# Kernel optimization log

Hardware: AMD Instinct MI355X
Metric: run time of the kernel (lower is better)

Reference implementation:

```python
import jax, jax.numpy as jnp
import numpy as np

DIM = 128
DEPTHS = 2
D_STATE = 16
D_CONV = 4
D_INNER = 2 * DIM          # expand=2
DT_RANK = DIM // 16        # ceil(128/16)=8


def layer_norm(x, g, b, eps=1e-5):
    mu = jnp.mean(x, axis=-1, keepdims=True)
    var = jnp.var(x, axis=-1, keepdims=True)
    return (x - mu) * jax.lax.rsqrt(var + eps) * g + b


def mamba_mixer(x, in_w, conv_w, conv_b, x_proj_w, dt_w, dt_b, A_log, Dp, out_w):
    # x: (B, L, DIM)
    Bb, L, _ = x.shape
    xz = x @ in_w                                  # (B, L, 2*D_INNER)
    xp, z = jnp.split(xz, 2, axis=-1)
    # causal depthwise conv1d over L (mamba: conv1d(padding=K-1)[..., :L])
    xpad = jnp.pad(xp, ((0, 0), (D_CONV - 1, 0), (0, 0)))
    xc = sum(xpad[:, k:k + L, :] * conv_w[:, k] for k in range(D_CONV)) + conv_b
    xc = jax.nn.silu(xc)
    x_dbl = xc @ x_proj_w                          # (B, L, DT_RANK + 2*D_STATE)
    dt = x_dbl[..., :DT_RANK]
    Bm = x_dbl[..., DT_RANK:DT_RANK + D_STATE]
    Cm = x_dbl[..., DT_RANK + D_STATE:]
    dt = jax.nn.softplus(dt @ dt_w + dt_b)         # (B, L, D_INNER)
    A = -jnp.exp(A_log)                            # (D_INNER, D_STATE)

    def step(h, inp):
        dt_t, B_t, C_t, x_t = inp                  # (B,di) (B,ds) (B,ds) (B,di)
        dA = jnp.exp(dt_t[:, :, None] * A)         # (B, di, ds)
        h = h * dA + (dt_t * x_t)[:, :, None] * B_t[:, None, :]
        y = jnp.einsum('bds,bs->bd', h, C_t)
        return h, y

    h0 = jnp.zeros((Bb, D_INNER, D_STATE), x.dtype)
    xs = (dt.transpose(1, 0, 2), Bm.transpose(1, 0, 2),
          Cm.transpose(1, 0, 2), xc.transpose(1, 0, 2))
    _, ys = jax.lax.scan(step, h0, xs)             # ys: (L, B, di)
    y = ys.transpose(1, 0, 2) + xc * Dp
    y = y * jax.nn.silu(z)
    return y @ out_w                               # (B, L, DIM)


def reference(x, skip, expand_w, pe_g, pe_b, ln_g, ln_b, in_proj_w, conv_w,
              conv_b, x_proj_w, dt_proj_w, dt_proj_b, A_log, D, out_proj_w,
              cbd_w, cbd_b):
    x = x.transpose(0, 2, 3, 1)                    # NCHW -> NHWC
    skip = skip.transpose(0, 2, 3, 1)
    # PatchExpanding: dim -> 2*dim, pixel-shuffle 2x2, LayerNorm(dim//2)
    B_, H, W, _ = x.shape
    x = x @ expand_w                               # (B, H, W, 2*DIM)
    c = x.shape[-1] // 4                           # = DIM//2
    x = x.reshape(B_, H, W, 2, 2, c).transpose(0, 1, 3, 2, 4, 5)
    x = x.reshape(B_, 2 * H, 2 * W, c)
    x = layer_norm(x, pe_g, pe_b)
    x = jnp.concatenate([x, skip], axis=-1)        # (B, 2H, 2W, DIM)
    B_, H2, W2, C = x.shape
    x = x.reshape(B_, H2 * W2, C)
    for i in range(DEPTHS):
        x = x + mamba_mixer(layer_norm(x, ln_g[i], ln_b[i]), in_proj_w[i],
                            conv_w[i], conv_b[i], x_proj_w[i], dt_proj_w[i],
                            dt_proj_b[i], A_log[i], D[i], out_proj_w[i])
    x = x @ cbd_w + cbd_b                          # (B, L, DIM//2)
    return x.reshape(B_, -1, H2, W2)               # faithful plain reshape (as torch .view)


def setup_inputs() -> dict:
    key = jax.random.key(0)
    ks = jax.random.split(key, 10)
    B, H, W = 2, 48, 48
    s = 0.02
    f32 = jnp.float32
    dt_init = float(np.log(np.expm1(0.01)))
    return {
        'x': jax.random.normal(ks[0], (B, DIM, H, W), f32),
        'skip': jax.random.normal(ks[1], (B, DIM // 2, 2 * H, 2 * W), f32),
        'expand_w': (jax.random.normal(ks[2], (DIM, 2 * DIM), f32) * s),
        'pe_g': jnp.ones((DIM // 2,), f32),
        'pe_b': jnp.zeros((DIM // 2,), f32),
        'ln_g': jnp.ones((DEPTHS, DIM), f32),
        'ln_b': jnp.zeros((DEPTHS, DIM), f32),
        'in_proj_w': jax.random.normal(ks[3], (DEPTHS, DIM, 2 * D_INNER), f32) * s,
        'conv_w': jax.random.normal(ks[4], (DEPTHS, D_INNER, D_CONV), f32) * 0.1,
        'conv_b': jnp.zeros((DEPTHS, D_INNER), f32),
        'x_proj_w': jax.random.normal(ks[5], (DEPTHS, D_INNER, DT_RANK + 2 * D_STATE), f32) * s,
        'dt_proj_w': jax.random.normal(ks[6], (DEPTHS, DT_RANK, D_INNER), f32) * 0.1,
        'dt_proj_b': jnp.full((DEPTHS, D_INNER), dt_init, f32),
        'A_log': jnp.log(jnp.broadcast_to(jnp.arange(1, D_STATE + 1, dtype=f32), (DEPTHS, D_INNER, D_STATE))),
        'D': jnp.ones((DEPTHS, D_INNER), f32),
        'out_proj_w': jax.random.normal(ks[7], (DEPTHS, D_INNER, DIM), f32) * s,
        'cbd_w': jax.random.normal(ks[8], (DIM, DIM // 2), f32) * s,
        'cbd_b': jnp.zeros((DIM // 2,), f32),
    }
```

## Files before the change

### kernel.cpp

```cpp
#include <hip/hip_runtime.h>
#include <hip/hip_bf16.h>

#define LB   9216
#define NB   2
#define ROWS (NB*LB)
#define NCH  576
#define CHL  16
#define NGRP 32

#define YST 264
#define LST 136

typedef __hip_bfloat16  bf16;
typedef __hip_bfloat162 bf162;
typedef __attribute__((ext_vector_type(8))) short short8;
typedef __attribute__((ext_vector_type(4))) float f32x4;

__device__ __forceinline__ float silu_f(float v) { return v / (1.f + __expf(-v)); }
__device__ __forceinline__ float softplus_f(float v) {
    return fmaxf(v, 0.f) + log1pf(__expf(-fabsf(v)));
}
__device__ __forceinline__ float ldm(const void* p, int j, bool bfm) {
    return bfm ? __bfloat162float(((const bf16*)p)[j]) : ((const float*)p)[j];
}
__device__ __forceinline__ void build_pw(float e1, float* pw) {
    float e2 = e1 * e1, e4 = e2 * e2, e8 = e4 * e4;
    pw[0] = e1;        pw[1] = e2;        pw[2] = e2 * e1;   pw[3] = e4;
    pw[4] = e4 * e1;   pw[5] = e4 * e2;   pw[6] = e4 * pw[2]; pw[7] = e8;
    pw[8] = e8 * e1;   pw[9] = e8 * e2;   pw[10] = e8 * pw[2]; pw[11] = e8 * e4;
    pw[12] = e8 * pw[4]; pw[13] = e8 * pw[5]; pw[14] = e8 * pw[6]; pw[15] = e8 * e8;
}
__device__ __forceinline__ bool load_astruct(const float* Atab, int dep, int d,
                                             float& A0, float* cs) {
    const f32x4* Ap = (const f32x4*)(Atab + dep * 4096 + d * 16);
    float A[16];
    #pragma unroll
    for (int i = 0; i < 4; ++i) {
        f32x4 v = Ap[i];
        A[4*i] = v[0]; A[4*i+1] = v[1]; A[4*i+2] = v[2]; A[4*i+3] = v[3];
    }
    A0 = A[0];
    bool structured = true;
    #pragma unroll
    for (int s = 0; s < 16; ++s) {
        cs[s] = A[s] - (float)(s + 1) * A0;
        structured = structured &&
            (fabsf(cs[s]) <= 0.03f * (float)(s + 1) * fabsf(A0) + 1e-6f);
    }
    return structured;
}

struct CvtArgs { const void* src[18]; int off[19]; };
#define PREP_CVT   274624
#define PREP_IPWT  131072
#define PREP_OPWT  65536
#define PREP_XPWT  24576
#define PREP_CBWT  8192
#define PREP_ATAB  8192
#define PREP_TOTAL (PREP_CVT + PREP_IPWT + PREP_OPWT + PREP_XPWT + PREP_CBWT + PREP_ATAB)
__global__ void k_prep(CvtArgs a, float* __restrict__ dst,
                       bf16* __restrict__ ipwT, bf16* __restrict__ opwT,
                       bf16* __restrict__ xpwT48, bf16* __restrict__ cbwT,
                       float* __restrict__ Atab) {
    int i = blockIdx.x * 256 + threadIdx.x;
    if (i >= PREP_TOTAL) return;
    bool bfm = (*(const unsigned int*)a.src[13]) != 0u;
    if (i < PREP_CVT) {
        int s = 0;
        while (i >= a.off[s + 1]) ++s;
        dst[i] = ldm(a.src[s], i - a.off[s], bfm);
    } else if (i < PREP_CVT + PREP_IPWT) {
        int j = i - PREP_CVT;
        int dep = j >> 16, r = j & 65535;
        int n = r >> 7, k = r & 127;
        ipwT[j] = __float2bfloat16(ldm(a.src[7], dep * 65536 + k * 512 + n, bfm));
    } else if (i < PREP_CVT + PREP_IPWT + PREP_OPWT) {
        int j = i - PREP_CVT - PREP_IPWT;
        int dep = j >> 15, r = j & 32767;
        int n = r >> 8, k = r & 255;
        opwT[j] = __float2bfloat16(ldm(a.src[15], dep * 32768 + k * 128 + n, bfm));
// ... 128 lines not shown
        const bf16* arow = &xsb[m * YST];
        f32x4 acc = (f32x4){0.f, 0.f, 0.f, 0.f};
        #pragma unroll
        for (int ks = 0; ks < 8; ++ks) {
            short8 av = *(const short8*)&arow[ks * 32 + quad * 8];
            short8 bv = *(const short8*)&wb[ks * 32 + quad * 8];
            acc = __builtin_amdgcn_mfma_f32_16x16x32_bf16(av, bv, acc, 0, 0, 0);
        }
        #pragma unroll
        for (int reg = 0; reg < 4; ++reg)
            xdbl[(quad * 4 + reg) * 48 + wv * 16 + m] = acc[reg];
    }
    __syncthreads();
    {
        float wj[8];
        #pragma unroll
        for (int j = 0; j < 8; ++j) wj[j] = dtw[dep * 2048 + j * 256 + t];
        float b0 = dtb[dep * 256 + t];
        #pragma unroll
        for (int r = 0; r < 16; ++r) {
            float a = b0;
            #pragma unroll
            for (int j = 0; j < 8; ++j) a += xdbl[r * 48 + j] * wj[j];
            dt[(size_t)(row0 + r) * 256 + t] = __float2bfloat16(softplus_f(a));
        }
    }
    {
        int r = t >> 4, s = t & 15;
        Bm[(size_t)(row0 + r) * 16 + s] = __float2bfloat16(xdbl[r * 48 + 8 + s]);
        Cm[(size_t)(row0 + r) * 16 + s] = __float2bfloat16(xdbl[r * 48 + 24 + s]);
    }
}

__global__ void k_scan1(const bf16* __restrict__ dt, const bf16* __restrict__ xc,
                        const bf16* __restrict__ Bm, const float* __restrict__ Atab,
                        bf16* __restrict__ hend, bf16* __restrict__ aprod,
                        int dep, int nch, int chl) {
    __shared__ __align__(16) float Bs[CHL * 16];
    int blk = blockIdx.x;
    int b = blk / nch, ch = blk - b * nch;
    int d = threadIdx.x;
    int rb = b * LB + ch * chl;
    {
        int r = d >> 4, c = d & 15;
        Bs[d] = __bfloat162float(Bm[(size_t)(rb + r) * 16 + c]);
    }
    __syncthreads();
    float A0, cs[16], h[16];
    bool structured = load_astruct(Atab, dep, d, A0, cs);
    #pragma unroll
    for (int s = 0; s < 16; ++s) h[s] = 0.f;
    float pd[4], px[4];
    #pragma unroll
    for (int i = 0; i < 4; ++i) {
        pd[i] = __bfloat162float(dt[(size_t)(rb + i) * 256 + d]);
        px[i] = __bfloat162float(xc[(size_t)(rb + i) * 256 + d]);
    }
    float sdt = 0.f;
    if (structured) {
        for (int t = 0; t < chl; ++t) {
            float dtv = pd[0], xv = px[0];
            pd[0] = pd[1]; pd[1] = pd[2]; pd[2] = pd[3];
            px[0] = px[1]; px[1] = px[2]; px[2] = px[3];
            int tn = t + 4;
            if (tn < chl) {
                pd[3] = __bfloat162float(dt[(size_t)(rb + tn) * 256 + d]);
                px[3] = __bfloat162float(xc[(size_t)(rb + tn) * 256 + d]);
            }
            sdt += dtv;
            float dtx = dtv * xv;
            float pw[16];
            build_pw(__expf(dtv * A0), pw);
            #pragma unroll
            for (int s = 0; s < 16; ++s) {
                float a = fmaf(pw[s], dtv * cs[s], pw[s]);
                h[s] = fmaf(h[s], a, dtx * Bs[t * 16 + s]);
            }
        }
    } else {
        for (int t = 0; t < chl; ++t) {
            float dtv = pd[0], xv = px[0];
            pd[0] = pd[1]; pd[1] = pd[2]; pd[2] = pd[3];
            px[0] = px[1]; px[1] = px[2]; px[2] = px[3];
            int tn = t + 4;
            if (tn < chl) {
                pd[3] = __bfloat162float(dt[(size_t)(rb + tn) * 256 + d]);
                px[3] = __bfloat162float(xc[(size_t)(rb + tn) * 256 + d]);
            }
            sdt += dtv;
            float dtx = dtv * xv;
            #pragma unroll
            for (int s = 0; s < 16; ++s) {
                float As = fmaf((float)(s + 1), A0, cs[s]);
                float a = __expf(dtv * As);
                h[s] = fmaf(h[s], a, dtx * Bs[t * 16 + s]);
            }
        }
    }
    size_t base = (size_t)blk * 4096 + (size_t)d * 16;
    float apv[16];
    if (structured) {
        float pw[16];
        build_pw(__expf(sdt * A0), pw);
        #pragma unroll
        for (int s = 0; s < 16; ++s) apv[s] = fmaf(pw[s], sdt * cs[s], pw[s]);
    } else {
        #pragma unroll
        for (int s = 0; s < 16; ++s) {
            float As = fmaf((float)(s + 1), A0, cs[s]);
            apv[s] = __expf(sdt * As);
        }
    }
    bf162* hp  = (bf162*)(hend + base);
    bf162* ap2 = (bf162*)(aprod + base);
    #pragma unroll
    for (int i = 0; i < 8; ++i) {
        bf162 hv; hv.x = __float2bfloat16(h[2*i]);   hv.y = __float2bfloat16(h[2*i+1]);
        bf162 av; av.x = __float2bfloat16(apv[2*i]); av.y = __float2bfloat16(apv[2*i+1]);
        hp[i]  = hv;
        ap2[i] = av;
    }
}

__global__ void k_scan2a(const bf16* __restrict__ hend, const bf16* __restrict__ aprod,
                         float* __restrict__ gA, float* __restrict__ gH,
                         int nch, int gsz) {
    int g = blockIdx.x >> 5;
    int p = (blockIdx.x & 31) * 256 + threadIdx.x;
    int b = p >> 12, rem = p & 4095;
    float ga = 1.f, gh = 0.f;
    int ch0 = g * gsz;
    for (int j = 0; j < gsz; ++j) {
        size_t idx = (size_t)(b * nch + ch0 + j) * 4096 + rem;
        float ap = __bfloat162float(aprod[idx]);
        float he = __bfloat162float(hend[idx]);
        gh = fmaf(gh, ap, he);
        ga *= ap;
    }
    gA[g * 8192 + p] = ga;
    gH[g * 8192 + p] = gh;
}

__global__ void k_scan2bc(bf16* __restrict__ hend, const bf16* __restrict__ aprod,
                          const float* __restrict__ gA, const float* __restrict__ gH,
                          int nch, int gsz) {
    int g = blockIdx.x >> 5;
    int p = (blockIdx.x & 31) * 256 + threadIdx.x;
    int b = p >> 12, rem = p & 4095;
    float h = 0.f;
    for (int gg = 0; gg < g; ++gg)
        h = fmaf(h, gA[gg * 8192 + p], gH[gg * 8192 + p]);
    int ch0 = g * gsz;
    for (int j = 0; j < gsz; ++j) {
        size_t idx = (size_t)(b * nch + ch0 + j) * 4096 + rem;
        float he = __bfloat162float(hend[idx]);
        float ap = __bfloat162float(aprod[idx]);
        hend[idx] = __float2bfloat16(h);
        h = fmaf(h, ap, he);
    }
}

__device__ __forceinline__ void scan3_core(const bf16* dt, const bf16* xc,
                                           const bf16* xz, const float* Atab,
                                           const float* Dp, const bf16* hstart,
                                           int dep, int blk, int row0, int d,
                                           const float* Bs, const float* Cs,
                                           bf16* ybuf) {
    size_t base = (size_t)blk * 4096 + (size_t)d * 16;
    float A0, cs[16], h[16];
    bool structured = load_astruct(Atab, dep, d, A0, cs);
    {
        const bf162* Hp = (const bf162*)(hstart + base);
        #pragma unroll
        for (int i = 0; i < 8; ++i) {
            bf162 v = Hp[i];
            h[2*i]   = __bfloat162float(v.x);
            h[2*i+1] = __bfloat162float(v.y);
        }
    }
    float Dv = Dp[dep * 256 + d];
    float pd[4], px[4], pz[4];
    #pragma unroll
    for (int i = 0; i < 4; ++i) {
        pd[i] = __bfloat162float(dt[(size_t)(row0 + i) * 256 + d]);
        px[i] = __bfloat162float(xc[(size_t)(row0 + i) * 256 + d]);
        pz[i] = __bfloat162float(xz[(size_t)(row0 + i) * 512 + 256 + d]);
    }
    if (structured) {
        #pragma unroll
        for (int r = 0; r < CHL; ++r) {
            float dtv = pd[0], xv = px[0], zv = pz[0];
            pd[0] = pd[1]; pd[1] = pd[2]; pd[2] = pd[3];
            px[0] = px[1]; px[1] = px[2]; px[2] = px[3];
            pz[0] = pz[1]; pz[1] = pz[2]; pz[2] = pz[3];
            int rn = r + 4;
            if (rn < CHL) {
                pd[3] = __bfloat162float(dt[(size_t)(row0 + rn) * 256 + d]);
                px[3] = __bfloat162float(xc[(size_t)(row0 + rn) * 256 + d]);
                pz[3] = __bfloat162float(xz[(size_t)(row0 + rn) * 512 + 256 + d]);
            }
            float dtx = dtv * xv;
            float y = 0.f;
            float pw[16];
            build_pw(__expf(dtv * A0), pw);
            #pragma unroll
            for (int s = 0; s < 16; ++s) {
                float a = fmaf(pw[s], dtv * cs[s], pw[s]);
                h[s] = fmaf(h[s], a, dtx * Bs[r * 16 + s]);
                y = fmaf(h[s], Cs[r * 16 + s], y);
            }
            y = (y + xv * Dv) * silu_f(zv);
            ybuf[r * YST + d] = __float2bfloat16(y);
        }
    } else {
        #pragma unroll
        for (int r = 0; r < CHL; ++r) {
            float dtv = pd[0], xv = px[0], zv = pz[0];
            pd[0] = pd[1]; pd[1] = pd[2]; pd[2] = pd[3];
            px[0] = px[1]; px[1] = px[2]; px[2] = px[3];
            pz[0] = pz[1]; pz[1] = pz[2]; pz[2] = pz[3];
            int rn = r + 4;
            if (rn < CHL) {
                pd[3] = __bfloat162float(dt[(size_t)(row0 + rn) * 256 + d]);
                px[3] = __bfloat162float(xc[(size_t)(row0 + rn) * 256 + d]);
                pz[3] = __bfloat162float(xz[(size_t)(row0 + rn) * 512 + 256 + d]);
            }
            float dtx = dtv * xv;
            float y = 0.f;
            #pragma unroll
            for (int s = 0; s < 16; ++s) {
                float As = fmaf((float)(s + 1), A0, cs[s]);
                float a = __expf(dtv * As);
                h[s] = fmaf(h[s], a, dtx * Bs[r * 16 + s]);
                y = fmaf(h[s], Cs[r * 16 + s], y);
            }
            y = (y + xv * Dv) * silu_f(zv);
            ybuf[r * YST + d] = __float2bfloat16(y);
        }
    }
}

__global__ __launch_bounds__(256, 4)
void k_scan3_out0(const bf16* __restrict__ dt, const bf16* __restrict__ xc,
                  const bf16* __restrict__ Bm, const bf16* __restrict__ Cm,
                  bf16* __restrict__ xz, const float* __restrict__ Atab,
                  const float* __restrict__ Dp, const bf16* __restrict__ hstart,
                  float* __restrict__ x0, const float* __restrict__ g,
                  const float* __restrict__ bb, const bf16* __restrict__ ipwT,
                  const bf16* __restrict__ opwT) {
    __shared__ float Bs[CHL * 16], Cs[CHL * 16];
    __shared__ bf16  ybuf[16 * YST];
    __shared__ float x0s[16 * 132];
    __shared__ bf16  lnt[16 * LST];
    int blk = blockIdx.x;
    int row0 = blk * 16;
    int t = threadIdx.x;
    {
        int r = t >> 4, c = t & 15;
        Bs[t] = __bfloat162float(Bm[(size_t)(row0 + r) * 16 + c]);
        Cs[t] = __bfloat162float(Cm[(size_t)(row0 + r) * 16 + c]);
    }
    for (int j = t; j < 2048; j += 256) {
        int r = j >> 7, c = j & 127;
        x0s[r * 132 + c] = x0[(size_t)row0 * 128 + j];
    }
    __syncthreads();
    scan3_core(dt, xc, xz, Atab, Dp, hstart, 0, blk, row0, t, Bs, Cs, ybuf);
    __syncthreads();
    int w = t >> 6, lane = t & 63;
    int m = lane & 15, quad = lane >> 4;
    {
        short8 av[8];
        #pragma unroll
        for (int ks = 0; ks < 8; ++ks)
            av[ks] = *(const short8*)&ybuf[m * YST + ks * 32 + quad * 8];
        #pragma unroll
        for (int j = 0; j < 2; ++j) {
            int nt = w * 2 + j;
            f32x4 acc = (f32x4){0.f, 0.f, 0.f, 0.f};
            #pragma unroll
            for (int ks = 0; ks < 8; ++ks) {
                short8 bv = *(const short8*)&opwT[(nt * 16 + m) * 256 + ks * 32 + quad * 8];
                acc = __builtin_amdgcn_mfma_f32_16x16x32_bf16(av[ks], bv, acc, 0, 0, 0);
            }
            #pragma unroll
            for (int reg = 0; reg < 4; ++reg)
                x0s[(quad * 4 + reg) * 132 + nt * 16 + m] += acc[reg];
        }
    }
    __syncthreads();
    for (int r = w; r < 16; r += 4) {
        float v0 = x0s[r * 132 + lane], v1 = x0s[r * 132 + 64 + lane];
        float s = v0 + v1, sq = v0 * v0 + v1 * v1;
        #pragma unroll
        for (int mm = 32; mm >= 1; mm >>= 1) { s += __shfl_xor(s, mm); sq += __shfl_xor(sq, mm); }
        float mu  = s * (1.f / 128.f);
        float var = sq * (1.f / 128.f) - mu * mu;
        float rs  = rsqrtf(var + 1e-5f);
        lnt[r * LST + lane]      = __float2bfloat16((v0 - mu) * rs * g[128 + lane] + bb[128 + lane]);
        lnt[r * LST + 64 + lane] = __float2bfloat16((v1 - mu) * rs * g[192 + lane] + bb[192 + lane]);
    }
    for (int j = t; j < 2048; j += 256) {
        int r = j >> 7, c = j & 127;
        x0[(size_t)row0 * 128 + j] = x0s[r * 132 + c];
    }
    __syncthreads();
    {
        short8 av2[4];
        #pragma unroll
        for (int ks = 0; ks < 4; ++ks)
            av2[ks] = *(const short8*)&lnt[m * LST + ks * 32 + quad * 8];
        const bf16* wb = ipwT + 65536;
        #pragma unroll
        for (int j = 0; j < 8; ++j) {
            int nt = w * 8 + j;
            f32x4 acc = (f32x4){0.f, 0.f, 0.f, 0.f};
            #pragma unroll
            for (int ks = 0; ks < 4; ++ks) {
                short8 bv = *(const short8*)&wb[(nt * 16 + m) * 128 + ks * 32 + quad * 8];
                acc = __builtin_amdgcn_mfma_f32_16x16x32_bf16(av2[ks], bv, acc, 0, 0, 0);
            }
            #pragma unroll
            for (int reg = 0; reg < 4; ++reg)
                xz[(size_t)(row0 + quad * 4 + reg) * 512 + nt * 16 + m] = __float2bfloat16(acc[reg]);
        }
    }
}

__global__ __launch_bounds__(256, 4)
void k_scan3_out1(const bf16* __restrict__ dt, const bf16* __restrict__ xc,
                  const bf16* __restrict__ Bm, const bf16* __restrict__ Cm,
                  bf16* __restrict__ xz, const float* __restrict__ Atab,
                  const float* __restrict__ Dp, const bf16* __restrict__ hstart,
                  const float* __restrict__ x0, const bf16* __restrict__ opwT,
                  const bf16* __restrict__ cbwT, const float* __restrict__ cbb,
                  void* __restrict__ out, const void* __restrict__ alog_raw) {
    __shared__ float Bs[CHL * 16], Cs[CHL * 16];
    __shared__ bf16  ybuf[16 * YST];
    __shared__ float x0s[16 * 132];
    __shared__ bf16  xfs[16 * LST];
    int blk = blockIdx.x;
    int row0 = blk * 16;
    int t = threadIdx.x;
    {
        int r = t >> 4, c = t & 15;
        Bs[t] = __bfloat162float(Bm[(size_t)(row0 + r) * 16 + c]);
        Cs[t] = __bfloat162float(Cm[(size_t)(row0 + r) * 16 + c]);
    }
    for (int j = t; j < 2048; j += 256) {
        int r = j >> 7, c = j & 127;
        x0s[r * 132 + c] = x0[(size_t)row0 * 128 + j];
    }
    __syncthreads();
    scan3_core(dt, xc, xz, Atab, Dp, hstart, 1, blk, row0, t, Bs, Cs, ybuf);
    __syncthreads();
    int w = t >> 6, lane = t & 63;
    int m = lane & 15, quad = lane >> 4;
    {
        short8 av[8];
        #pragma unroll
        for (int ks = 0; ks < 8; ++ks)
            av[ks] = *(const short8*)&ybuf[m * YST + ks * 32 + quad * 8];
        const bf16* wb = opwT + 32768;
        #pragma unroll
        for (int j = 0; j < 2; ++j) {
            int nt = w * 2 + j;
            f32x4 acc = (f32x4){0.f, 0.f, 0.f, 0.f};
            #pragma unroll
            for (int ks = 0; ks < 8; ++ks) {
                short8 bv = *(const short8*)&wb[(nt * 16 + m) * 256 + ks * 32 + quad * 8];
                acc = __builtin_amdgcn_mfma_f32_16x16x32_bf16(av[ks], bv, acc, 0, 0, 0);
            }
            #pragma unroll
            for (int reg = 0; reg < 4; ++reg) {
                int lr  = quad * 4 + reg;
                int col = nt * 16 + m;
                xfs[lr * LST + col] = __float2bfloat16(x0s[lr * 132 + col] + acc[reg]);
            }
        }
    }
    __syncthreads();
    {
        short8 av2[4];
        #pragma unroll
        for (int ks = 0; ks < 4; ++ks)
            av2[ks] = *(const short8*)&xfs[m * LST + ks * 32 + quad * 8];
        bool bfm = (*(const unsigned int*)alog_raw) != 0u;
// ... 14 lines not shown
            else     ((float*)out)[idx] = v;
        }
    }
}

extern "C" void kernel_launch(void* const* d_in, const int* in_sizes, int n_in,
                              void* d_out, int out_size, void* d_ws, size_t ws_size,
                              hipStream_t stream) {
    (void)in_sizes; (void)n_in; (void)out_size; (void)ws_size;
    static const int sz[18] = {0, 0, 32768, 64, 64, 256, 256, 131072,
                               2048, 512, 20480, 4096, 512, 8192, 512, 65536, 8192, 64};
    CvtArgs ca;
    int off = 0;
    for (int i = 0; i < 18; ++i) { ca.src[i] = d_in[i]; ca.off[i] = off; off += sz[i]; }
    ca.off[18] = off;

    float* wf     = (float*)d_ws;
    bf16*  ipwT   = (bf16*)(wf + PREP_CVT);
    bf16*  opwT   = ipwT + PREP_IPWT;
    bf16*  xpwT48 = opwT + PREP_OPWT;
    bf16*  cbwT   = xpwT48 + PREP_XPWT;
    float* Atab   = (float*)(cbwT + PREP_CBWT);
    float* x0     = Atab + PREP_ATAB;
    bf16*  xz     = (bf16*)(x0 + (size_t)ROWS * 128);
    bf16*  xc     = xz + (size_t)ROWS * 512;
    bf16*  dt     = xc + (size_t)ROWS * 256;
    bf16*  Bm     = dt + (size_t)ROWS * 256;
    bf16*  Cm     = Bm + (size_t)ROWS * 16;
    bf16*  hend   = Cm + (size_t)ROWS * 16;
    bf16*  aprod  = hend + (size_t)NB * NCH * 4096;
    float* gA     = (float*)(aprod + (size_t)NB * NCH * 4096);
    float* gH     = gA + NGRP * 8192;

    int gsz = NCH / NGRP;

    const float* ew   = wf + ca.off[2];
    const float* peg  = wf + ca.off[3];
    const float* peb  = wf + ca.off[4];
    const float* lng  = wf + ca.off[5];
    const float* lnb  = wf + ca.off[6];
    const float* cw   = wf + ca.off[8];
    const float* cb   = wf + ca.off[9];
    const float* dtw  = wf + ca.off[11];
    const float* dtb  = wf + ca.off[12];
    const float* Dp   = wf + ca.off[14];
    const float* cbb  = wf + ca.off[17];

    k_prep   <<<(PREP_TOTAL + 255) / 256, 256, 0, stream>>>(ca, wf, ipwT, opwT, xpwT48, cbwT, Atab);
    k_expand <<<NB * 48 * 48, 256, 0, stream>>>(d_in[0], d_in[1], ew, peg, peb, x0, d_in[13]);
    k_lngemm_in<<<ROWS / 16, 256, 0, stream>>>(x0, lng, lnb, ipwT, xz, 0);
    for (int dep = 0; dep < 2; ++dep) {
        k_convxp <<<ROWS / 16, 256, 0, stream>>>(xz, cw, cb, xpwT48, dtw, dtb, xc, dt, Bm, Cm, dep);
        k_scan1  <<<NB * NCH, 256, 0, stream>>>(dt, xc, Bm, Atab, hend, aprod, dep, NCH, CHL);
        k_scan2a <<<NGRP * 32, 256, 0, stream>>>(hend, aprod, gA, gH, NCH, gsz);
        k_scan2bc<<<NGRP * 32, 256, 0, stream>>>(hend, aprod, gA, gH, NCH, gsz);
        if (dep == 0)
            k_scan3_out0<<<ROWS / 16, 256, 0, stream>>>(dt, xc, Bm, Cm, xz, Atab, Dp, hend,
                                                        x0, lng, lnb, ipwT, opwT);
        else
            k_scan3_out1<<<ROWS / 16, 256, 0, stream>>>(dt, xc, Bm, Cm, xz, Atab, Dp, hend,
                                                        x0, opwT, cbwT, cbb, d_out, d_in[13]);
    }
}
```

Baseline: 353.4 us.

## Stage scan inputs in shared memory with vector loads and batch scan2 loads

The scan1 and scan3 kernels now copy each chunk's dt, xc and z slices into shared memory with 16-byte vector loads, replacing per-thread strided scalar global loads with a rolling prefetch. The time loops are fully unrolled and read B and C through vectorized LDS reads. The scan2 kernels load all GSZ chunk values up front to expose memory-level parallelism, and the hend/aprod/x0 reads and writes use wide vector accesses. Shared memory is reused between the staging and x0 buffers, which raises per-block LDS usage and register pressure and may lower occupancy.

Measured after the change: 449.7 us. 27.2% more time.

```diff
diff --git a/kernel.cpp b/kernel.cpp
--- a/kernel.cpp
+++ b/kernel.cpp
@@ -7,6 +7,7 @@
 #define NCH  576
 #define CHL  16
 #define NGRP 32
+#define GSZ  18
 
 #define YST 264
 #define LST 136
@@ -22,6 +23,12 @@
 }
 __device__ __forceinline__ float ldm(const void* p, int j, bool bfm) {
     return bfm ? __bfloat162float(((const bf16*)p)[j]) : ((const float*)p)[j];
+}
+__device__ __forceinline__ short8 pack_bf8(const float* v) {
+    union { short8 s; bf16 b[8]; } u;
+    #pragma unroll
+    for (int i = 0; i < 8; ++i) u.b[i] = __float2bfloat16(v[i]);
+    return u.s;
 }
 __device__ __forceinline__ void build_pw(float e1, float* pw) {
     float e2 = e1 * e1, e4 = e2 * e2, e8 = e4 * e4;
@@ -240,68 +247,79 @@
     }
 }
 
-__global__ void k_scan1(const bf16* __restrict__ dt, const bf16* __restrict__ xc,
-                        const bf16* __restrict__ Bm, const float* __restrict__ Atab,
-                        bf16* __restrict__ hend, bf16* __restrict__ aprod,
-                        int dep, int nch, int chl) {
-    __shared__ __align__(16) float Bs[CHL * 16];
+__global__ __launch_bounds__(256, 4)
+void k_scan1(const bf16* __restrict__ dt, const bf16* __restrict__ xc,
+             const bf16* __restrict__ Bm, const float* __restrict__ Atab,
+             bf16* __restrict__ hend, bf16* __restrict__ aprod,
+             int dep, int nch, int chl) {
+    (void)chl;
+    __shared__ __align__(16) char smem[1024 + 8192 + 8192];
+    float* Bs  = (float*)smem;
+    bf16*  dts = (bf16*)(smem + 1024);
+    bf16*  xcs = (bf16*)(smem + 1024 + 8192);
     int blk = blockIdx.x;
     int b = blk / nch, ch = blk - b * nch;
     int d = threadIdx.x;
-    int rb = b * LB + ch * chl;
+    int rb = b * LB + ch * CHL;
     {
         int r = d >> 4, c = d & 15;
         Bs[d] = __bfloat162float(Bm[(size_t)(rb + r) * 16 + c]);
     }
+    {
+        const short8* g1 = (const short8*)(dt + (size_t)rb * 256);
+        const short8* g2 = (const short8*)(xc + (size_t)rb * 256);
+        short8* s1 = (short8*)dts;
+        short8* s2 = (short8*)xcs;
+        s1[d] = g1[d]; s1[d + 256] = g1[d + 256];
+        s2[d] = g2[d]; s2[d + 256] = g2[d + 256];
+    }
     __syncthreads();
     float A0, cs[16], h[16];
     bool structured = load_astruct(Atab, dep, d, A0, cs);
     #pragma unroll
     for (int s = 0; s < 16; ++s) h[s] = 0.f;
-    float pd[4], px[4];
-    #pragma unroll
-    for (int i = 0; i < 4; ++i) {
-        pd[i] = __bfloat162float(dt[(size_t)(rb + i) * 256 + d]);
-        px[i] = __bfloat162float(xc[(size_t)(rb + i) * 256 + d]);
-    }
     float sdt = 0.f;
     if (structured) {
-        for (int t = 0; t < chl; ++t) {
-            float dtv = pd[0], xv = px[0];
-            pd[0] = pd[1]; pd[1] = pd[2]; pd[2] = pd[3];
-            px[0] = px[1]; px[1] = px[2]; px[2] = px[3];
-            int tn = t + 4;
-            if (tn < chl) {
-                pd[3] = __bfloat162float(dt[(size_t)(rb + tn) * 256 + d]);
-                px[3] = __bfloat162float(xc[(size_t)(rb + tn) * 256 + d]);
-            }
+        #pragma unroll
+        for (int t = 0; t < CHL; ++t) {
+            float dtv = __bfloat162float(dts[t * 256 + d]);
+            float xv  = __bfloat162float(xcs[t * 256 + d]);
             sdt += dtv;
             float dtx = dtv * xv;
+            float Bv[16];
+            const f32x4* Bp = (const f32x4*)&Bs[t * 16];
+            #pragma unroll
+            for (int i = 0; i < 4; ++i) {
+                f32x4 v = Bp[i];
+                Bv[4*i] = v[0]; Bv[4*i+1] = v[1]; Bv[4*i+2] = v[2]; Bv[4*i+3] = v[3];
+            }
             float pw[16];
             build_pw(__expf(dtv * A0), pw);
             #pragma unroll
             for (int s = 0; s < 16; ++s) {
                 float a = fmaf(pw[s], dtv * cs[s], pw[s]);
-                h[s] = fmaf(h[s], a, dtx * Bs[t * 16 + s]);
+                h[s] = fmaf(h[s], a, dtx * Bv[s]);
             }
         }
     } else {
-        for (int t = 0; t < chl; ++t) {
-            float dtv = pd[0], xv = px[0];
-            pd[0] = pd[1]; pd[1] = pd[2]; pd[2] = pd[3];
-            px[0] = px[1]; px[1] = px[2]; px[2] = px[3];
-            int tn = t + 4;
-            if (tn < chl) {
-                pd[3] = __bfloat162float(dt[(size_t)(rb + tn) * 256 + d]);
-                px[3] = __bfloat162float(xc[(size_t)(rb + tn) * 256 + d]);
-            }
+        #pragma unroll
+        for (int t = 0; t < CHL; ++t) {
+            float dtv = __bfloat162float(dts[t * 256 + d]);
+            float xv  = __bfloat162float(xcs[t * 256 + d]);
             sdt += dtv;
             float dtx = dtv * xv;
+            float Bv[16];
+            const f32x4* Bp = (const f32x4*)&Bs[t * 16];
+            #pragma unroll
+            for (int i = 0; i < 4; ++i) {
+                f32x4 v = Bp[i];
+                Bv[4*i] = v[0]; Bv[4*i+1] = v[1]; Bv[4*i+2] = v[2]; Bv[4*i+3] = v[3];
+            }
             #pragma unroll
             for (int s = 0; s < 16; ++s) {
                 float As = fmaf((float)(s + 1), A0, cs[s]);
                 float a = __expf(dtv * As);
-                h[s] = fmaf(h[s], a, dtx * Bs[t * 16 + s]);
+                h[s] = fmaf(h[s], a, dtx * Bv[s]);
             }
         }
     }
@@ -319,31 +337,30 @@
             apv[s] = __expf(sdt * As);
         }
     }
-    bf162* hp  = (bf162*)(hend + base);
-    bf162* ap2 = (bf162*)(aprod + base);
-    #pragma unroll
-    for (int i = 0; i < 8; ++i) {
-        bf162 hv; hv.x = __float2bfloat16(h[2*i]);   hv.y = __float2bfloat16(h[2*i+1]);
-        bf162 av; av.x = __float2bfloat16(apv[2*i]); av.y = __float2bfloat16(apv[2*i+1]);
-        hp[i]  = hv;
-        ap2[i] = av;
-    }
+    *(short8*)(hend + base)      = pack_bf8(h);
+    *(short8*)(hend + base + 8)  = pack_bf8(h + 8);
+    *(short8*)(aprod + base)     = pack_bf8(apv);
+    *(short8*)(aprod + base + 8) = pack_bf8(apv + 8);
 }
 
 __global__ void k_scan2a(const bf16* __restrict__ hend, const bf16* __restrict__ aprod,
-                         float* __restrict__ gA, float* __restrict__ gH,
-                         int nch, int gsz) {
+                         float* __restrict__ gA, float* __restrict__ gH, int nch) {
     int g = blockIdx.x >> 5;
     int p = (blockIdx.x & 31) * 256 + threadIdx.x;
     int b = p >> 12, rem = p & 4095;
+    int ch0 = g * GSZ;
+    size_t base = (size_t)(b * nch + ch0) * 4096 + rem;
+    float ap[GSZ], he[GSZ];
+    #pragma unroll
+    for (int j = 0; j < GSZ; ++j) {
+        ap[j] = __bfloat162float(aprod[base + (size_t)j * 4096]);
+        he[j] = __bfloat162float(hend[base + (size_t)j * 4096]);
+    }
     float ga = 1.f, gh = 0.f;
-    int ch0 = g * gsz;
-    for (int j = 0; j < gsz; ++j) {
-        size_t idx = (size_t)(b * nch + ch0 + j) * 4096 + rem;
-        float ap = __bfloat162float(aprod[idx]);
-        float he = __bfloat162float(hend[idx]);
-        gh = fmaf(gh, ap, he);
-        ga *= ap;
+    #pragma unroll
+    for (int j = 0; j < GSZ; ++j) {
+        gh = fmaf(gh, ap[j], he[j]);
+        ga *= ap[j];
     }
     gA[g * 8192 + p] = ga;
     gH[g * 8192 + p] = gh;
@@ -351,71 +368,72 @@
 
 __global__ void k_scan2bc(bf16* __restrict__ hend, const bf16* __restrict__ aprod,
                           const float* __restrict__ gA, const float* __restrict__ gH,
-                          int nch, int gsz) {
+                          int nch) {
     int g = blockIdx.x >> 5;
     int p = (blockIdx.x & 31) * 256 + threadIdx.x;
     int b = p >> 12, rem = p & 4095;
     float h = 0.f;
     for (int gg = 0; gg < g; ++gg)
         h = fmaf(h, gA[gg * 8192 + p], gH[gg * 8192 + p]);
-    int ch0 = g * gsz;
-    for (int j = 0; j < gsz; ++j) {
-        size_t idx = (size_t)(b * nch + ch0 + j) * 4096 + rem;
-        float he = __bfloat162float(hend[idx]);
-        float ap = __bfloat162float(aprod[idx]);
-        hend[idx] = __float2bfloat16(h);
-        h = fmaf(h, ap, he);
-    }
-}
-
-__device__ __forceinline__ void scan3_core(const bf16* dt, const bf16* xc,
-                                           const bf16* xz, const float* Atab,
+    int ch0 = g * GSZ;
+    size_t base = (size_t)(b * nch + ch0) * 4096 + rem;
+    float ap[GSZ], he[GSZ];
+    #pragma unroll
+    for (int j = 0; j < GSZ; ++j) {
+        ap[j] = __bfloat162float(aprod[base + (size_t)j * 4096]);
+        he[j] = __bfloat162float(hend[base + (size_t)j * 4096]);
+    }
+    #pragma unroll
+    for (int j = 0; j < GSZ; ++j) {
+        hend[base + (size_t)j * 4096] = __float2bfloat16(h);
+        h = fmaf(h, ap[j], he[j]);
+    }
+}
+
+__device__ __forceinline__ void scan3_core(const bf16* dts, const bf16* xcs,
+                                           const bf16* zs, const float* Atab,
                                            const float* Dp, const bf16* hstart,
-                                           int dep, int blk, int row0, int d,
+                                           int dep, int blk, int d,
                                            const float* Bs, const float* Cs,
                                            bf16* ybuf) {
     size_t base = (size_t)blk * 4096 + (size_t)d * 16;
     float A0, cs[16], h[16];
     bool structured = load_astruct(Atab, dep, d, A0, cs);
     {
-        const bf162* Hp = (const bf162*)(hstart + base);
+        union { short8 s; bf16 b[8]; } u0, u1;
+        u0.s = *(const short8*)(hstart + base);
+        u1.s = *(const short8*)(hstart + base + 8);
         #pragma unroll
         for (int i = 0; i < 8; ++i) {
-            bf162 v = Hp[i];
-            h[2*i]   = __bfloat162float(v.x);
-            h[2*i+1] = __bfloat162float(v.y);
+            h[i]     = __bfloat162float(u0.b[i]);
+            h[8 + i] = __bfloat162float(u1.b[i]);
         }
     }
     float Dv = Dp[dep * 256 + d];
-    float pd[4], px[4], pz[4];
-    #pragma unroll
-    for (int i = 0; i < 4; ++i) {
-        pd[i] = __bfloat162float(dt[(size_t)(row0 + i) * 256 + d]);
-        px[i] = __bfloat162float(xc[(size_t)(row0 + i) * 256 + d]);
-        pz[i] = __bfloat162float(xz[(size_t)(row0 + i) * 512 + 256 + d]);
-    }
     if (structured) {
         #pragma unroll
         for (int r = 0; r < CHL; ++r) {
-            float dtv = pd[0], xv = px[0], zv = pz[0];
-            pd[0] = pd[1]; pd[1] = pd[2]; pd[2] = pd[3];
-            px[0] = px[1]; px[1] = px[2]; px[2] = px[3];
-            pz[0] = pz[1]; pz[1] = pz[2]; pz[2] = pz[3];
-            int rn = r + 4;
-            if (rn < CHL) {
-                pd[3] = __bfloat162float(dt[(size_t)(row0 + rn) * 256 + d]);
-                px[3] = __bfloat162float(xc[(size_t)(row0 + rn) * 256 + d]);
-                pz[3] = __bfloat162float(xz[(size_t)(row0 + rn) * 512 + 256 + d]);
-            }
+            float dtv = __bfloat162float(dts[r * 256 + d]);
+            float xv  = __bfloat162float(xcs[r * 256 + d]);
+            float zv  = __bfloat162float(zs[r * 256 + d]);
             float dtx = dtv * xv;
+            float Bv[16], Cv[16];
+            const f32x4* Bp = (const f32x4*)&Bs[r * 16];
+            const f32x4* Cp = (const f32x4*)&Cs[r * 16];
+            #pragma unroll
+            for (int i = 0; i < 4; ++i) {
+                f32x4 v = Bp[i], w = Cp[i];
+                Bv[4*i] = v[0]; Bv[4*i+1] = v[1]; Bv[4*i+2] = v[2]; Bv[4*i+3] = v[3];
+                Cv[4*i] = w[0]; Cv[4*i+1] = w[1]; Cv[4*i+2] = w[2]; Cv[4*i+3] = w[3];
+            }
             float y = 0.f;
             float pw[16];
             build_pw(__expf(dtv * A0), pw);
             #pragma unroll
             for (int s = 0; s < 16; ++s) {
                 float a = fmaf(pw[s], dtv * cs[s], pw[s]);
-                h[s] = fmaf(h[s], a, dtx * Bs[r * 16 + s]);
-                y = fmaf(h[s], Cs[r * 16 + s], y);
+                h[s] = fmaf(h[s], a, dtx * Bv[s]);
+                y = fmaf(h[s], Cv[s], y);
             }
             y = (y + xv * Dv) * silu_f(zv);
             ybuf[r * YST + d] = __float2bfloat16(y);
@@ -423,28 +441,47 @@
     } else {
         #pragma unroll
         for (int r = 0; r < CHL; ++r) {
-            float dtv = pd[0], xv = px[0], zv = pz[0];
-            pd[0] = pd[1]; pd[1] = pd[2]; pd[2] = pd[3];
-            px[0] = px[1]; px[1] = px[2]; px[2] = px[3];
-            pz[0] = pz[1]; pz[1] = pz[2]; pz[2] = pz[3];
-            int rn = r + 4;
-            if (rn < CHL) {
-                pd[3] = __bfloat162float(dt[(size_t)(row0 + rn) * 256 + d]);
-                px[3] = __bfloat162float(xc[(size_t)(row0 + rn) * 256 + d]);
-                pz[3] = __bfloat162float(xz[(size_t)(row0 + rn) * 512 + 256 + d]);
-            }
+            float dtv = __bfloat162float(dts[r * 256 + d]);
+            float xv  = __bfloat162float(xcs[r * 256 + d]);
+            float zv  = __bfloat162float(zs[r * 256 + d]);
             float dtx = dtv * xv;
+            float Bv[16], Cv[16];
+            const f32x4* Bp = (const f32x4*)&Bs[r * 16];
+            const f32x4* Cp = (const f32x4*)&Cs[r * 16];
+            #pragma unroll
+            for (int i = 0; i < 4; ++i) {
+                f32x4 v = Bp[i], w = Cp[i];
+                Bv[4*i] = v[0]; Bv[4*i+1] = v[1]; Bv[4*i+2] = v[2]; Bv[4*i+3] = v[3];
+                Cv[4*i] = w[0]; Cv[4*i+1] = w[1]; Cv[4*i+2] = w[2]; Cv[4*i+3] = w[3];
+            }
             float y = 0.f;
             #pragma unroll
             for (int s = 0; s < 16; ++s) {
                 float As = fmaf((float)(s + 1), A0, cs[s]);
                 float a = __expf(dtv * As);
-                h[s] = fmaf(h[s], a, dtx * Bs[r * 16 + s]);
-                y = fmaf(h[s], Cs[r * 16 + s], y);
+                h[s] = fmaf(h[s], a, dtx * Bv[s]);
+                y = fmaf(h[s], Cv[s], y);
             }
             y = (y + xv * Dv) * silu_f(zv);
             ybuf[r * YST + d] = __float2bfloat16(y);
         }
+    }
+}
+
+__device__ __forceinline__ void stage_scan3(const bf16* dt, const bf16* xc,
+                                            const bf16* xz, int row0, int t,
+                                            bf16* dts, bf16* xcs, bf16* zs) {
+    const short8* g1 = (const short8*)(dt + (size_t)row0 * 256);
+    const short8* g2 = (const short8*)(xc + (size_t)row0 * 256);
+    short8* s1 = (short8*)dts;
+    short8* s2 = (short8*)xcs;
+    s1[t] = g1[t]; s1[t + 256] = g1[t + 256];
+    s2[t] = g2[t]; s2[t + 256] = g2[t + 256];
+    #pragma unroll
+    for (int k = 0; k < 2; ++k) {
+        int v = t + k * 256;
+        int r = v >> 5, d8 = v & 31;
+        ((short8*)zs)[v] = *(const short8*)&xz[(size_t)(row0 + r) * 512 + 256 + d8 * 8];
     }
 }
 
@@ -456,24 +493,39 @@
                   float* __restrict__ x0, const float* __restrict__ g,
                   const float* __restrict__ bb, const bf16* __restrict__ ipwT,
                   const bf16* __restrict__ opwT) {
-    __shared__ float Bs[CHL * 16], Cs[CHL * 16];
-    __shared__ bf16  ybuf[16 * YST];
-    __shared__ float x0s[16 * 132];
-    __shared__ bf16  lnt[16 * LST];
+    __shared__ __align__(16) char smem[2048 + 16 * YST * 2 + 24576];
+    float* Bs  = (float*)smem;
+    float* Cs  = (float*)(smem + 1024);
+    bf16*  ybuf= (bf16*)(smem + 2048);
+    char*  stg = smem + 2048 + 16 * YST * 2;
+    bf16*  dts = (bf16*)stg;
+    bf16*  xcs = (bf16*)(stg + 8192);
+    bf16*  zs  = (bf16*)(stg + 16384);
+    float* x0s = (float*)stg;
+    bf16*  lnt = (bf16*)(stg + 8448);
     int blk = blockIdx.x;
     int row0 = blk * 16;
     int t = threadIdx.x;
+    f32x4 rx0[2];
+    {
+        const f32x4* gx = (const f32x4*)(x0 + (size_t)row0 * 128);
+        rx0[0] = gx[t]; rx0[1] = gx[t + 256];
+    }
     {
         int r = t >> 4, c = t & 15;
         Bs[t] = __bfloat162float(Bm[(size_t)(row0 + r) * 16 + c]);
         Cs[t] = __bfloat162float(Cm[(size_t)(row0 + r) * 16 + c]);
     }
-    for (int j = t; j < 2048; j += 256) {
-        int r = j >> 7, c = j & 127;
-        x0s[r * 132 + c] = x0[(size_t)row0 * 128 + j];
-    }
-    __syncthreads();
-    scan3_core(dt, xc, xz, Atab, Dp, hstart, 0, blk, row0, t, Bs, Cs, ybuf);
+    stage_scan3(dt, xc, xz, row0, t, dts, xcs, zs);
+    __syncthreads();
+    scan3_core(dts, xcs, zs, Atab, Dp, hstart, 0, blk, t, Bs, Cs, ybuf);
+    __syncthreads();
+    #pragma unroll
+    for (int k = 0; k < 2; ++k) {
+        int v = t + k * 256;
+        int r = v >> 5, c4 = v & 31;
+        *(f32x4*)&x0s[r * 132 + c4 * 4] = rx0[k];
+    }
     __syncthreads();
     int w = t >> 6, lane = t & 63;
     int m = lane & 15, quad = lane >> 4;
@@ -508,9 +560,11 @@
         lnt[r * LST + lane]      = __float2bfloat16((v0 - mu) * rs * g[128 + lane] + bb[128 + lane]);
         lnt[r * LST + 64 + lane] = __float2bfloat16((v1 - mu) * rs * g[192 + lane] + bb[192 + lane]);
     }
-    for (int j = t; j < 2048; j += 256) {
-        int r = j >> 7, c = j & 127;
-        x0[(size_t)row0 * 128 + j] = x0s[r * 132 + c];
+    #pragma unroll
+    for (int k = 0; k < 2; ++k) {
+        int v = t + k * 256;
+        int r = v >> 5, c4 = v & 31;
+        ((f32x4*)(x0 + (size_t)row0 * 128))[v] = *(const f32x4*)&x0s[r * 132 + c4 * 4];
     }
     __syncthreads();
     {
@@ -543,24 +597,39 @@
                   const float* __restrict__ x0, const bf16* __restrict__ opwT,
                   const bf16* __restrict__ cbwT, const float* __restrict__ cbb,
                   void* __restrict__ out, const void* __restrict__ alog_raw) {
-    __shared__ float Bs[CHL * 16], Cs[CHL * 16];
-    __shared__ bf16  ybuf[16 * YST];
-    __shared__ float x0s[16 * 132];
-    __shared__ bf16  xfs[16 * LST];
+    __shared__ __align__(16) char smem[2048 + 16 * YST * 2 + 24576];
+    float* Bs  = (float*)smem;
+    float* Cs  = (float*)(smem + 1024);
+    bf16*  ybuf= (bf16*)(smem + 2048);
+    char*  stg = smem + 2048 + 16 * YST * 2;
+    bf16*  dts = (bf16*)stg;
+    bf16*  xcs = (bf16*)(stg + 8192);
+    bf16*  zs  = (bf16*)(stg + 16384);
+    float* x0s = (float*)stg;
+    bf16*  xfs = (bf16*)(stg + 8448);
     int blk = blockIdx.x;
     int row0 = blk * 16;
     int t = threadIdx.x;
+    f32x4 rx0[2];
+    {
+        const f32x4* gx = (const f32x4*)(x0 + (size_t)row0 * 128);
+        rx0[0] = gx[t]; rx0[1] = gx[t + 256];
+    }
     {
         int r = t >> 4, c = t & 15;
         Bs[t] = __bfloat162float(Bm[(size_t)(row0 + r) * 16 + c]);
         Cs[t] = __bfloat162float(Cm[(size_t)(row0 + r) * 16 + c]);
     }
-    for (int j = t; j < 2048; j += 256) {
-        int r = j >> 7, c = j & 127;
-        x0s[r * 132 + c] = x0[(size_t)row0 * 128 + j];
-    }
-    __syncthreads();
-    scan3_core(dt, xc, xz, Atab, Dp, hstart, 1, blk, row0, t, Bs, Cs, ybuf);
+    stage_scan3(dt, xc, xz, row0, t, dts, xcs, zs);
+    __syncthreads();
+    scan3_core(dts, xcs, zs, Atab, Dp, hstart, 1, blk, t, Bs, Cs, ybuf);
+    __syncthreads();
+    #pragma unroll
+    for (int k = 0; k < 2; ++k) {
+        int v = t + k * 256;
+        int r = v >> 5, c4 = v & 31;
+        *(f32x4*)&x0s[r * 132 + c4 * 4] = rx0[k];
+    }
     __syncthreads();
     int w = t >> 6, lane = t & 63;
     int m = lane & 15, quad = lane >> 4;
@@ -641,8 +710,6 @@
     float* gA     = (float*)(aprod + (size_t)NB * NCH * 4096);
     float* gH     = gA + NGRP * 8192;
 
-    int gsz = NCH / NGRP;
-
     const float* ew   = wf + ca.off[2];
     const float* peg  = wf + ca.off[3];
     const float* peb  = wf + ca.off[4];
@@ -661,8 +728,8 @@
     for (int dep = 0; dep < 2; ++dep) {
         k_convxp <<<ROWS / 16, 256, 0, stream>>>(xz, cw, cb, xpwT48, dtw, dtb, xc, dt, Bm, Cm, dep);
         k_scan1  <<<NB * NCH, 256, 0, stream>>>(dt, xc, Bm, Atab, hend, aprod, dep, NCH, CHL);
-        k_scan2a <<<NGRP * 32, 256, 0, stream>>>(hend, aprod, gA, gH, NCH, gsz);
-        k_scan2bc<<<NGRP * 32, 256, 0, stream>>>(hend, aprod, gA, gH, NCH, gsz);
+        k_scan2a <<<NGRP * 32, 256, 0, stream>>>(hend, aprod, gA, gH, NCH);
+        k_scan2bc<<<NGRP * 32, 256, 0, stream>>>(hend, aprod, gA, gH, NCH);
         if (dep == 0)
             k_scan3_out0<<<ROWS / 16, 256, 0, stream>>>(dt, xc, Bm, Cm, xz, Atab, Dp, hend,
                                                         x0, lng, lnb, ipwT, opwT);
```

## Use packed float2 math in scan kernels and unroll chunk-combine loads

Applied to the files above, without the earlier changes.

Rewrites the per-state recurrence in scan1 and scan3 on two-wide float vectors so the compiler can emit packed FP32 multiply/FMA instructions, halving the instruction count of the inner state loop. The chunk-combine kernels get a compile-time group size, so all 18 loads are issued up front before the dependent FMA chain. hend/aprod stores and hstart loads are widened to 16-byte accesses. The costs are higher register pressure from the unrolled load arrays and a reliance on the compiler actually emitting packed ops.

New measurement: 347.6 us. No clear change (-1.7%).

```diff
diff --git a/kernel.cpp b/kernel.cpp
--- a/kernel.cpp
+++ b/kernel.cpp
@@ -7,6 +7,7 @@
 #define NCH  576
 #define CHL  16
 #define NGRP 32
+#define GSZ  18
 
 #define YST 264
 #define LST 136
@@ -15,6 +16,7 @@
 typedef __hip_bfloat162 bf162;
 typedef __attribute__((ext_vector_type(8))) short short8;
 typedef __attribute__((ext_vector_type(4))) float f32x4;
+typedef __attribute__((ext_vector_type(2))) float f32x2;
 
 __device__ __forceinline__ float silu_f(float v) { return v / (1.f + __expf(-v)); }
 __device__ __forceinline__ float softplus_f(float v) {
@@ -23,15 +25,28 @@
 __device__ __forceinline__ float ldm(const void* p, int j, bool bfm) {
     return bfm ? __bfloat162float(((const bf16*)p)[j]) : ((const float*)p)[j];
 }
-__device__ __forceinline__ void build_pw(float e1, float* pw) {
-    float e2 = e1 * e1, e4 = e2 * e2, e8 = e4 * e4;
-    pw[0] = e1;        pw[1] = e2;        pw[2] = e2 * e1;   pw[3] = e4;
-    pw[4] = e4 * e1;   pw[5] = e4 * e2;   pw[6] = e4 * pw[2]; pw[7] = e8;
-    pw[8] = e8 * e1;   pw[9] = e8 * e2;   pw[10] = e8 * pw[2]; pw[11] = e8 * e4;
-    pw[12] = e8 * pw[4]; pw[13] = e8 * pw[5]; pw[14] = e8 * pw[6]; pw[15] = e8 * e8;
-}
-__device__ __forceinline__ bool load_astruct(const float* Atab, int dep, int d,
-                                             float& A0, float* cs) {
+__device__ __forceinline__ short8 pack_bf8(const float* v) {
+    union { short8 s; bf16 b[8]; } u;
+    #pragma unroll
+    for (int i = 0; i < 8; ++i) u.b[i] = __float2bfloat16(v[i]);
+    return u.s;
+}
+__device__ __forceinline__ void build_pw2(float e1, f32x2* pw2) {
+    float e2 = e1 * e1;
+    f32x2 M2 = (f32x2){e2, e2};
+    f32x2 M4 = M2 * M2;
+    f32x2 M8 = M4 * M4;
+    pw2[0] = (f32x2){e1, e2};
+    pw2[1] = pw2[0] * M2;
+    pw2[2] = pw2[0] * M4;
+    pw2[3] = pw2[1] * M4;
+    pw2[4] = pw2[0] * M8;
+    pw2[5] = pw2[1] * M8;
+    pw2[6] = pw2[2] * M8;
+    pw2[7] = pw2[3] * M8;
+}
+__device__ __forceinline__ bool load_astruct2(const float* Atab, int dep, int d,
+                                              float& A0, f32x2* cs2) {
     const f32x4* Ap = (const f32x4*)(Atab + dep * 4096 + d * 16);
     float A[16];
     #pragma unroll
@@ -43,9 +58,10 @@
     bool structured = true;
     #pragma unroll
     for (int s = 0; s < 16; ++s) {
-        cs[s] = A[s] - (float)(s + 1) * A0;
+        float c = A[s] - (float)(s + 1) * A0;
         structured = structured &&
-            (fabsf(cs[s]) <= 0.03f * (float)(s + 1) * fabsf(A0) + 1e-6f);
+            (fabsf(c) <= 0.03f * (float)(s + 1) * fabsf(A0) + 1e-6f);
+        cs2[s >> 1][s & 1] = c;
     }
     return structured;
 }
@@ -254,10 +270,11 @@
         Bs[d] = __bfloat162float(Bm[(size_t)(rb + r) * 16 + c]);
     }
     __syncthreads();
-    float A0, cs[16], h[16];
-    bool structured = load_astruct(Atab, dep, d, A0, cs);
-    #pragma unroll
-    for (int s = 0; s < 16; ++s) h[s] = 0.f;
+    float A0;
+    f32x2 cs2[8], h2[8];
+    bool structured = load_astruct2(Atab, dep, d, A0, cs2);
+    #pragma unroll
+    for (int i = 0; i < 8; ++i) h2[i] = (f32x2){0.f, 0.f};
     float pd[4], px[4];
     #pragma unroll
     for (int i = 0; i < 4; ++i) {
@@ -277,12 +294,14 @@
             }
             sdt += dtv;
             float dtx = dtv * xv;
-            float pw[16];
-            build_pw(__expf(dtv * A0), pw);
-            #pragma unroll
-            for (int s = 0; s < 16; ++s) {
-                float a = fmaf(pw[s], dtv * cs[s], pw[s]);
-                h[s] = fmaf(h[s], a, dtx * Bs[t * 16 + s]);
+            f32x2 pw2[8];
+            build_pw2(__expf(dtv * A0), pw2);
+            f32x2 dtv2 = (f32x2){dtv, dtv}, dtx2 = (f32x2){dtx, dtx};
+            const f32x2* Bp2 = (const f32x2*)&Bs[t * 16];
+            #pragma unroll
+            for (int i = 0; i < 8; ++i) {
+                f32x2 a = pw2[i] * (dtv2 * cs2[i]) + pw2[i];
+                h2[i] = h2[i] * a + dtx2 * Bp2[i];
             }
         }
     } else {
@@ -299,51 +318,56 @@
             float dtx = dtv * xv;
             #pragma unroll
             for (int s = 0; s < 16; ++s) {
-                float As = fmaf((float)(s + 1), A0, cs[s]);
+                float As = fmaf((float)(s + 1), A0, cs2[s >> 1][s & 1]);
                 float a = __expf(dtv * As);
-                h[s] = fmaf(h[s], a, dtx * Bs[t * 16 + s]);
+                h2[s >> 1][s & 1] = fmaf(h2[s >> 1][s & 1], a, dtx * Bs[t * 16 + s]);
             }
         }
     }
     size_t base = (size_t)blk * 4096 + (size_t)d * 16;
-    float apv[16];
+    float hv[16], apv[16];
+    #pragma unroll
+    for (int i = 0; i < 8; ++i) { hv[2*i] = h2[i][0]; hv[2*i+1] = h2[i][1]; }
     if (structured) {
-        float pw[16];
-        build_pw(__expf(sdt * A0), pw);
-        #pragma unroll
-        for (int s = 0; s < 16; ++s) apv[s] = fmaf(pw[s], sdt * cs[s], pw[s]);
+        f32x2 pw2[8];
+        build_pw2(__expf(sdt * A0), pw2);
+        f32x2 sdt2 = (f32x2){sdt, sdt};
+        #pragma unroll
+        for (int i = 0; i < 8; ++i) {
+            f32x2 ap = pw2[i] * (sdt2 * cs2[i]) + pw2[i];
+            apv[2*i] = ap[0]; apv[2*i+1] = ap[1];
+        }
     } else {
         #pragma unroll
         for (int s = 0; s < 16; ++s) {
-            float As = fmaf((float)(s + 1), A0, cs[s]);
+            float As = fmaf((float)(s + 1), A0, cs2[s >> 1][s & 1]);
             apv[s] = __expf(sdt * As);
         }
     }
-    bf162* hp  = (bf162*)(hend + base);
-    bf162* ap2 = (bf162*)(aprod + base);
-    #pragma unroll
-    for (int i = 0; i < 8; ++i) {
-        bf162 hv; hv.x = __float2bfloat16(h[2*i]);   hv.y = __float2bfloat16(h[2*i+1]);
-        bf162 av; av.x = __float2bfloat16(apv[2*i]); av.y = __float2bfloat16(apv[2*i+1]);
-        hp[i]  = hv;
-        ap2[i] = av;
-    }
+    *(short8*)(hend + base)      = pack_bf8(hv);
+    *(short8*)(hend + base + 8)  = pack_bf8(hv + 8);
+    *(short8*)(aprod + base)     = pack_bf8(apv);
+    *(short8*)(aprod + base + 8) = pack_bf8(apv + 8);
 }
 
 __global__ void k_scan2a(const bf16* __restrict__ hend, const bf16* __restrict__ aprod,
-                         float* __restrict__ gA, float* __restrict__ gH,
-                         int nch, int gsz) {
+                         float* __restrict__ gA, float* __restrict__ gH, int nch) {
     int g = blockIdx.x >> 5;
     int p = (blockIdx.x & 31) * 256 + threadIdx.x;
     int b = p >> 12, rem = p & 4095;
+    int ch0 = g * GSZ;
+    size_t base = (size_t)(b * nch + ch0) * 4096 + rem;
+    float ap[GSZ], he[GSZ];
+    #pragma unroll
+    for (int j = 0; j < GSZ; ++j) {
+        ap[j] = __bfloat162float(aprod[base + (size_t)j * 4096]);
+        he[j] = __bfloat162float(hend[base + (size_t)j * 4096]);
+    }
     float ga = 1.f, gh = 0.f;
-    int ch0 = g * gsz;
-    for (int j = 0; j < gsz; ++j) {
-        size_t idx = (size_t)(b * nch + ch0 + j) * 4096 + rem;
-        float ap = __bfloat162float(aprod[idx]);
-        float he = __bfloat162float(hend[idx]);
-        gh = fmaf(gh, ap, he);
-        ga *= ap;
+    #pragma unroll
+    for (int j = 0; j < GSZ; ++j) {
+        gh = fmaf(gh, ap[j], he[j]);
+        ga *= ap[j];
     }
     gA[g * 8192 + p] = ga;
     gH[g * 8192 + p] = gh;
@@ -351,20 +375,25 @@
 
 __global__ void k_scan2bc(bf16* __restrict__ hend, const bf16* __restrict__ aprod,
                           const float* __restrict__ gA, const float* __restrict__ gH,
-                          int nch, int gsz) {
+                          int nch) {
     int g = blockIdx.x >> 5;
     int p = (blockIdx.x & 31) * 256 + threadIdx.x;
     int b = p >> 12, rem = p & 4095;
     float h = 0.f;
     for (int gg = 0; gg < g; ++gg)
         h = fmaf(h, gA[gg * 8192 + p], gH[gg * 8192 + p]);
-    int ch0 = g * gsz;
-    for (int j = 0; j < gsz; ++j) {
-        size_t idx = (size_t)(b * nch + ch0 + j) * 4096 + rem;
-        float he = __bfloat162float(hend[idx]);
-        float ap = __bfloat162float(aprod[idx]);
-        hend[idx] = __float2bfloat16(h);
-        h = fmaf(h, ap, he);
+    int ch0 = g * GSZ;
+    size_t base = (size_t)(b * nch + ch0) * 4096 + rem;
+    float ap[GSZ], he[GSZ];
+    #pragma unroll
+    for (int j = 0; j < GSZ; ++j) {
+        ap[j] = __bfloat162float(aprod[base + (size_t)j * 4096]);
+        he[j] = __bfloat162float(hend[base + (size_t)j * 4096]);
+    }
+    #pragma unroll
+    for (int j = 0; j < GSZ; ++j) {
+        hend[base + (size_t)j * 4096] = __float2bfloat16(h);
+        h = fmaf(h, ap[j], he[j]);
     }
 }
 
@@ -375,15 +404,17 @@
                                            const float* Bs, const float* Cs,
                                            bf16* ybuf) {
     size_t base = (size_t)blk * 4096 + (size_t)d * 16;
-    float A0, cs[16], h[16];
-    bool structured = load_astruct(Atab, dep, d, A0, cs);
-    {
-        const bf162* Hp = (const bf162*)(hstart + base);
-        #pragma unroll
-        for (int i = 0; i < 8; ++i) {
-            bf162 v = Hp[i];
-            h[2*i]   = __bfloat162float(v.x);
-            h[2*i+1] = __bfloat162float(v.y);
+    float A0;
+    f32x2 cs2[8], h2[8];
+    bool structured = load_astruct2(Atab, dep, d, A0, cs2);
+    {
+        union { short8 s; bf16 b[8]; } u0, u1;
+        u0.s = *(const short8*)(hstart + base);
+        u1.s = *(const short8*)(hstart + base + 8);
+        #pragma unroll
+        for (int i = 0; i < 4; ++i) {
+            h2[i]     = (f32x2){__bfloat162float(u0.b[2*i]), __bfloat162float(u0.b[2*i+1])};
+            h2[4 + i] = (f32x2){__bfloat162float(u1.b[2*i]), __bfloat162float(u1.b[2*i+1])};
         }
     }
     float Dv = Dp[dep * 256 + d];
@@ -408,15 +439,19 @@
                 pz[3] = __bfloat162float(xz[(size_t)(row0 + rn) * 512 + 256 + d]);
             }
             float dtx = dtv * xv;
-            float y = 0.f;
-            float pw[16];
-            build_pw(__expf(dtv * A0), pw);
-            #pragma unroll
-            for (int s = 0; s < 16; ++s) {
-                float a = fmaf(pw[s], dtv * cs[s], pw[s]);
-                h[s] = fmaf(h[s], a, dtx * Bs[r * 16 + s]);
-                y = fmaf(h[s], Cs[r * 16 + s], y);
-            }
+            f32x2 pw2[8];
+            build_pw2(__expf(dtv * A0), pw2);
+            f32x2 dtv2 = (f32x2){dtv, dtv}, dtx2 = (f32x2){dtx, dtx};
+            f32x2 y2 = (f32x2){0.f, 0.f};
+            const f32x2* Bp2 = (const f32x2*)&Bs[r * 16];
+            const f32x2* Cp2 = (const f32x2*)&Cs[r * 16];
+            #pragma unroll
+            for (int i = 0; i < 8; ++i) {
+                f32x2 a = pw2[i] * (dtv2 * cs2[i]) + pw2[i];
+                h2[i] = h2[i] * a + dtx2 * Bp2[i];
+                y2 = h2[i] * Cp2[i] + y2;
+            }
+            float y = y2[0] + y2[1];
             y = (y + xv * Dv) * silu_f(zv);
             ybuf[r * YST + d] = __float2bfloat16(y);
         }
@@ -437,10 +472,11 @@
             float y = 0.f;
             #pragma unroll
             for (int s = 0; s < 16; ++s) {
-                float As = fmaf((float)(s + 1), A0, cs[s]);
+                float As = fmaf((float)(s + 1), A0, cs2[s >> 1][s & 1]);
                 float a = __expf(dtv * As);
-                h[s] = fmaf(h[s], a, dtx * Bs[r * 16 + s]);
-                y = fmaf(h[s], Cs[r * 16 + s], y);
+                float hv = fmaf(h2[s >> 1][s & 1], a, dtx * Bs[r * 16 + s]);
+                h2[s >> 1][s & 1] = hv;
+                y = fmaf(hv, Cs[r * 16 + s], y);
             }
             y = (y + xv * Dv) * silu_f(zv);
             ybuf[r * YST + d] = __float2bfloat16(y);
@@ -456,7 +492,7 @@
                   float* __restrict__ x0, const float* __restrict__ g,
                   const float* __restrict__ bb, const bf16* __restrict__ ipwT,
                   const bf16* __restrict__ opwT) {
-    __shared__ float Bs[CHL * 16], Cs[CHL * 16];
+    __shared__ __align__(16) float Bs[CHL * 16], Cs[CHL * 16];
     __shared__ bf16  ybuf[16 * YST];
     __shared__ float x0s[16 * 132];
     __shared__ bf16  lnt[16 * LST];
@@ -543,7 +579,7 @@
                   const float* __restrict__ x0, const bf16* __restrict__ opwT,
                   const bf16* __restrict__ cbwT, const float* __restrict__ cbb,
                   void* __restrict__ out, const void* __restrict__ alog_raw) {
-    __shared__ float Bs[CHL * 16], Cs[CHL * 16];
+    __shared__ __align__(16) float Bs[CHL * 16], Cs[CHL * 16];
     __shared__ bf16  ybuf[16 * YST];
     __shared__ float x0s[16 * 132];
     __shared__ bf16  xfs[16 * LST];
@@ -641,8 +677,6 @@
     float* gA     = (float*)(aprod + (size_t)NB * NCH * 4096);
     float* gH     = gA + NGRP * 8192;
 
-    int gsz = NCH / NGRP;
-
     const float* ew   = wf + ca.off[2];
     const float* peg  = wf + ca.off[3];
     const float* peb  = wf + ca.off[4];
@@ -661,8 +695,8 @@
     for (int dep = 0; dep < 2; ++dep) {
         k_convxp <<<ROWS / 16, 256, 0, stream>>>(xz, cw, cb, xpwT48, dtw, dtb, xc, dt, Bm, Cm, dep);
         k_scan1  <<<NB * NCH, 256, 0, stream>>>(dt, xc, Bm, Atab, hend, aprod, dep, NCH, CHL);
-        k_scan2a <<<NGRP * 32, 256, 0, stream>>>(hend, aprod, gA, gH, NCH, gsz);
-        k_scan2bc<<<NGRP * 32, 256, 0, stream>>>(hend, aprod, gA, gH, NCH, gsz);
+        k_scan2a <<<NGRP * 32, 256, 0, stream>>>(hend, aprod, gA, gH, NCH);
+        k_scan2bc<<<NGRP * 32, 256, 0, stream>>>(hend, aprod, gA, gH, NCH);
         if (dep == 0)
             k_scan3_out0<<<ROWS / 16, 256, 0, stream>>>(dt, xc, Bm, Cm, xz, Atab, Dp, hend,
                                                         x0, lng, lnb, ipwT, opwT);
```
